# Kernel tuning notes

Measured on AMD Instinct MI355X. Metric: run time of the kernel, lower is better.

Reference implementation:

```python
import jax, jax.numpy as jnp
import numpy as np

LAM = 0.95

def setup_inputs() -> dict:
    key = jax.random.key(0)
    d2 = jax.random.normal(key, (16, 8192, 256), dtype=jnp.float32)
    return {"d2": d2}

def reference(d2) -> jnp.ndarray:
    # z_t = lam * z_{t-1} + (1 - lam) * d2_t, scanned over time axis L
    B, L, K = d2.shape
    lam = jnp.asarray(LAM, d2.dtype)
    one_minus = jnp.asarray(1.0 - LAM, d2.dtype)

    def step(z, x):  # z: [B,K], x: [B,K]
        z = lam * z + one_minus * x
        return z, z

    z0 = jnp.zeros((B, K), dtype=d2.dtype)
    _, z = jax.lax.scan(step, z0, jnp.swapaxes(d2, 0, 1))  # [L,B,K]
    return jnp.swapaxes(z, 0, 1)  # [B,L,K]
```

## Files before the change

kernel.cpp:

```cpp
#include <hip/hip_runtime.h>


#define LAM   0.95f
#define CHUNK 128
#define WARM  128
#define UNROLL 8

typedef float v4f __attribute__((ext_vector_type(4)));

constexpr int B  = 16;
constexpr int L  = 8192;
constexpr int K  = 256;
constexpr int G  = L / CHUNK;
constexpr int S4 = K / 4;

__global__ __launch_bounds__(256) void ewma_kernel(const float* __restrict__ x,
                                                   float* __restrict__ out) {
    const int gw   = (int)((blockIdx.x * 256u + threadIdx.x) >> 6);
    const int lane = threadIdx.x & 63;
    const int b    = gw >> 6;
    const int j    = gw & 63;
    const int s    = j * CHUNK;
    const int t0   = (j == 0) ? 0 : (s - WARM);

    const long chanoff = (long)b * L * K + (long)lane * 4;
    const v4f* __restrict__ pin  = (const v4f*)(x   + chanoff) + (long)t0 * S4;
    v4f*       __restrict__ pout = (v4f*)      (out + chanoff) + (long)t0 * S4;

    const float c = 1.0f - LAM;
    v4f z = {0.f, 0.f, 0.f, 0.f};

    const int total      = (s + CHUNK) - t0;
    const int tiles      = total / UNROLL;
    const int warm_tiles = (s - t0) / UNROLL;

    v4f bufA[UNROLL], bufB[UNROLL];

    auto load_tile = [&](v4f (&buf)[UNROLL], int t) {
        const v4f* __restrict__ p = pin + (long)t * UNROLL * S4;
        #pragma unroll
        for (int u = 0; u < UNROLL; ++u) buf[u] = p[(long)u * S4];
    };

    auto comp_tile = [&](v4f (&buf)[UNROLL], int t) {
        v4f* __restrict__ p = pout + (long)t * UNROLL * S4;
        const bool st = (t >= warm_tiles);
        #pragma unroll
        for (int u = 0; u < UNROLL; ++u) {
            const v4f xv = buf[u];
            z.x = fmaf(LAM, z.x, c * xv.x);
            z.y = fmaf(LAM, z.y, c * xv.y);
            z.z = fmaf(LAM, z.z, c * xv.z);
            z.w = fmaf(LAM, z.w, c * xv.w);
            if (st) __builtin_nontemporal_store(z, &p[(long)u * S4]);
        }
    };

    load_tile(bufA, 0);
    for (int t = 0; t < tiles; t += 2) {
        load_tile(bufB, t + 1);
        comp_tile(bufA, t);
        if (t + 2 < tiles) load_tile(bufA, t + 2);
        comp_tile(bufB, t + 1);
    }
}

extern "C" void kernel_launch(void* const* d_in, const int* in_sizes, int n_in,
                              void* d_out, int out_size, void* d_ws, size_t ws_size,
                              hipStream_t stream) {
    const float* x = (const float*)d_in[0];
    float* out = (float*)d_out;

    const int total_waves = B * G;
    const int blocks = total_waves / 4;
    hipLaunchKernelGGL(ewma_kernel, dim3(blocks), dim3(256), 0, stream, x, out);
}
```

Before: 248.4 us.

## Map one channel per thread with scalar loads and four times more blocks

Replaces the float4-per-lane layout, where one wave covered all 256 channels of a chunk, with scalar per-thread channels. Each block of four waves now covers all 256 channels for one (batch, chunk) pair, so the grid grows from 256 to 1024 blocks. The unroll depth doubles to 16 so more loads are in flight per thread. This should raise occupancy and memory-level parallelism, at the cost of narrower 4-byte accesses instead of 16-byte vector accesses.

```diff
diff --git a/kernel.cpp b/kernel.cpp
--- a/kernel.cpp
+++ b/kernel.cpp
@@ -4,55 +4,49 @@
 #define LAM   0.95f
 #define CHUNK 128
 #define WARM  128
-#define UNROLL 8
-
-typedef float v4f __attribute__((ext_vector_type(4)));
+#define UNROLL 16
 
 constexpr int B  = 16;
 constexpr int L  = 8192;
 constexpr int K  = 256;
 constexpr int G  = L / CHUNK;
-constexpr int S4 = K / 4;
+constexpr int KS = 4;
 
 __global__ __launch_bounds__(256) void ewma_kernel(const float* __restrict__ x,
                                                    float* __restrict__ out) {
-    const int gw   = (int)((blockIdx.x * 256u + threadIdx.x) >> 6);
+    const int wib  = (int)(threadIdx.x >> 6);
     const int lane = threadIdx.x & 63;
-    const int b    = gw >> 6;
-    const int j    = gw & 63;
+    const int j    = blockIdx.x & (G - 1);
+    const int b    = blockIdx.x >> 6;
     const int s    = j * CHUNK;
     const int t0   = (j == 0) ? 0 : (s - WARM);
 
-    const long chanoff = (long)b * L * K + (long)lane * 4;
-    const v4f* __restrict__ pin  = (const v4f*)(x   + chanoff) + (long)t0 * S4;
-    v4f*       __restrict__ pout = (v4f*)      (out + chanoff) + (long)t0 * S4;
+    const long chan = (long)b * L * K + wib * 64 + lane;
+    const float* __restrict__ pin  = x   + chan + (long)t0 * K;
+    float*       __restrict__ pout = out + chan + (long)t0 * K;
 
     const float c = 1.0f - LAM;
-    v4f z = {0.f, 0.f, 0.f, 0.f};
+    float z = 0.f;
 
     const int total      = (s + CHUNK) - t0;
     const int tiles      = total / UNROLL;
     const int warm_tiles = (s - t0) / UNROLL;
 
-    v4f bufA[UNROLL], bufB[UNROLL];
+    float bufA[UNROLL], bufB[UNROLL];
 
-    auto load_tile = [&](v4f (&buf)[UNROLL], int t) {
-        const v4f* __restrict__ p = pin + (long)t * UNROLL * S4;
+    auto load_tile = [&](float (&buf)[UNROLL], int t) {
+        const float* __restrict__ p = pin + (long)t * UNROLL * K;
         #pragma unroll
-        for (int u = 0; u < UNROLL; ++u) buf[u] = p[(long)u * S4];
+        for (int u = 0; u < UNROLL; ++u) buf[u] = p[(long)u * K];
     };
 
-    auto comp_tile = [&](v4f (&buf)[UNROLL], int t) {
-        v4f* __restrict__ p = pout + (long)t * UNROLL * S4;
+    auto comp_tile = [&](float (&buf)[UNROLL], int t) {
+        float* __restrict__ p = pout + (long)t * UNROLL * K;
         const bool st = (t >= warm_tiles);
         #pragma unroll
         for (int u = 0; u < UNROLL; ++u) {
-            const v4f xv = buf[u];
-            z.x = fmaf(LAM, z.x, c * xv.x);
-            z.y = fmaf(LAM, z.y, c * xv.y);
-            z.z = fmaf(LAM, z.z, c * xv.z);
-            z.w = fmaf(LAM, z.w, c * xv.w);
-            if (st) __builtin_nontemporal_store(z, &p[(long)u * S4]);
+            z = fmaf(LAM, z, c * buf[u]);
+            if (st) __builtin_nontemporal_store(z, &p[(long)u * K]);
         }
     };
 
@@ -71,7 +65,6 @@
     const float* x = (const float*)d_in[0];
     float* out = (float*)d_out;
 
-    const int total_waves = B * G;
-    const int blocks = total_waves / 4;
+    const int blocks = B * G;
     hipLaunchKernelGGL(ewma_kernel, dim3(blocks), dim3(256), 0, stream, x, out);
 }
```

Result: no change. 249.6 us (+0.5%).

## Stream input through a per-wave LDS ring with async global-to-LDS loads

Applied to the files above, without the earlier changes.

Replaces the register double-buffered tile loop with a 32-row LDS ring per wave, filled by asynchronous global_load_lds transfers. Up to 31 rows stay in flight, and manual vmcnt waits let each step consume one row while issuing the next. The goal is far more outstanding memory requests per wave for this bandwidth-bound scan, since each CU runs only a few waves. In exchange it uses 128KB of LDS per block, hand-counted vmcnt values that depend on store ordering, and plain stores instead of nontemporal ones.

```diff
diff --git a/kernel.cpp b/kernel.cpp
--- a/kernel.cpp
+++ b/kernel.cpp
@@ -1,67 +1,87 @@
 #include <hip/hip_runtime.h>
 
 
-#define LAM   0.95f
+#define LAM  0.95f
 #define CHUNK 128
 #define WARM  128
-#define UNROLL 8
+#define RING  32
 
 typedef float v4f __attribute__((ext_vector_type(4)));
+typedef const __attribute__((address_space(1))) unsigned int gu32;
+typedef __attribute__((address_space(3)))       unsigned int lu32;
 
-constexpr int B  = 16;
-constexpr int L  = 8192;
-constexpr int K  = 256;
-constexpr int G  = L / CHUNK;
+constexpr int B = 16;
+constexpr int L = 8192;
+constexpr int K = 256;
+constexpr int G = L / CHUNK;
 constexpr int S4 = K / 4;
+
+#define WAITV(N)                                                   \
+    do {                                                           \
+        asm volatile("s_waitcnt vmcnt(" #N ")" ::: "memory");      \
+        __builtin_amdgcn_sched_barrier(0);                         \
+    } while (0)
 
 __global__ __launch_bounds__(256) void ewma_kernel(const float* __restrict__ x,
                                                    float* __restrict__ out) {
-    const int gw   = (int)((blockIdx.x * 256u + threadIdx.x) >> 6);
+    __shared__ float lds[4][RING][K];
+
+    const int wib  = (int)(threadIdx.x >> 6);
     const int lane = threadIdx.x & 63;
+    const int gw   = (int)(blockIdx.x * 4u) + wib;
     const int b    = gw >> 6;
-    const int j    = gw & 63;
+    const int j    = gw & (G - 1);
     const int s    = j * CHUNK;
     const int t0   = (j == 0) ? 0 : (s - WARM);
 
-    const long chanoff = (long)b * L * K + (long)lane * 4;
-    const v4f* __restrict__ pin  = (const v4f*)(x   + chanoff) + (long)t0 * S4;
-    v4f*       __restrict__ pout = (v4f*)      (out + chanoff) + (long)t0 * S4;
+    const int total = (s + CHUNK) - t0;
+    const int warm  = s - t0;
+
+    const float* __restrict__ prow = x + (long)b * L * K + (long)t0 * K;
+    v4f* __restrict__ pout = (v4f*)(out + (long)b * L * K + (long)lane * 4)
+                             + (long)t0 * S4;
 
     const float c = 1.0f - LAM;
     v4f z = {0.f, 0.f, 0.f, 0.f};
 
-    const int total      = (s + CHUNK) - t0;
-    const int tiles      = total / UNROLL;
-    const int warm_tiles = (s - t0) / UNROLL;
-
-    v4f bufA[UNROLL], bufB[UNROLL];
-
-    auto load_tile = [&](v4f (&buf)[UNROLL], int t) {
-        const v4f* __restrict__ p = pin + (long)t * UNROLL * S4;
-        #pragma unroll
-        for (int u = 0; u < UNROLL; ++u) buf[u] = p[(long)u * S4];
+    auto stage = [&](int t) {
+        const float* src = prow + (long)t * K + lane * 4;
+        lu32* dst = (lu32*)&lds[wib][t & (RING - 1)][0];
+        __builtin_amdgcn_global_load_lds((gu32*)src, dst, 16, 0, 0);
     };
 
-    auto comp_tile = [&](v4f (&buf)[UNROLL], int t) {
-        v4f* __restrict__ p = pout + (long)t * UNROLL * S4;
-        const bool st = (t >= warm_tiles);
-        #pragma unroll
-        for (int u = 0; u < UNROLL; ++u) {
-            const v4f xv = buf[u];
-            z.x = fmaf(LAM, z.x, c * xv.x);
-            z.y = fmaf(LAM, z.y, c * xv.y);
-            z.z = fmaf(LAM, z.z, c * xv.z);
-            z.w = fmaf(LAM, z.w, c * xv.w);
-            if (st) __builtin_nontemporal_store(z, &p[(long)u * S4]);
-        }
+    auto consume = [&](int t) {
+        const v4f xv = *(const v4f*)&lds[wib][t & (RING - 1)][lane * 4];
+        z.x = fmaf(LAM, z.x, c * xv.x);
+        z.y = fmaf(LAM, z.y, c * xv.y);
+        z.z = fmaf(LAM, z.z, c * xv.z);
+        z.w = fmaf(LAM, z.w, c * xv.w);
+        if (t >= warm) pout[(long)t * S4] = z;
     };
 
-    load_tile(bufA, 0);
-    for (int t = 0; t < tiles; t += 2) {
-        load_tile(bufB, t + 1);
-        comp_tile(bufA, t);
-        if (t + 2 < tiles) load_tile(bufA, t + 2);
-        comp_tile(bufB, t + 1);
+    #pragma unroll 1
+    for (int t = 0; t < RING - 1; ++t) stage(t);
+
+    const int s1e = warm + RING;
+    const int s2e = total - RING + 1;
+
+    int t = 0;
+    #pragma unroll 1
+    for (; t < s1e; ++t) {
+        WAITV(30);
+        consume(t);
+        stage(t + RING - 1);
+    }
+    #pragma unroll 1
+    for (; t < s2e; ++t) {
+        WAITV(60);
+        consume(t);
+        stage(t + RING - 1);
+    }
+    #pragma unroll 1
+    for (; t < total; ++t) {
+        WAITV(30);
+        consume(t);
     }
 }
 
@@ -71,7 +91,6 @@
     const float* x = (const float*)d_in[0];
     float* out = (float*)d_out;
 
-    const int total_waves = B * G;
-    const int blocks = total_waves / 4;
+    const int blocks = (B * G) / 4;
     hipLaunchKernelGGL(ewma_kernel, dim3(blocks), dim3(256), 0, stream, x, out);
 }
```

New measurement: 254.2 us. 2.3% more time.
